# Performance work log

Measured on AMD Instinct MI355X. Metric: run time of the kernel, lower is better.

## Reference

```python
import jax, jax.numpy as jnp
import numpy as np

B, N, C, L, E = 8, 8192, 256, 4, 131072  # graphs, nodes/graph, channels (in=hidden=out), layers, edges/graph


def setup_inputs() -> dict:
    key = jax.random.key(0)
    ks = jax.random.split(key, 9)
    batch_node_tsr = jax.random.normal(ks[0], (B, N, C), jnp.float32)
    edge_index = jax.random.randint(ks[1], (B, 2, E), 0, N, jnp.int32)
    batch_last_node_idx_list = jnp.arange(1, B + 1, dtype=jnp.int32) * N - 1
    s1 = 1.0 / np.sqrt(C)
    s2 = 1.0 / np.sqrt(2 * C)
    # Base GraphConv layers: out = x @ Wr.T + sum_nbr(x) @ Wn.T + b  (all CxC since in=hidden=out)
    base_Wr = jax.random.uniform(ks[2], (L, C, C), jnp.float32, -s1, s1)
    base_Wn = jax.random.uniform(ks[3], (L, C, C), jnp.float32, -s1, s1)
    base_b = jax.random.uniform(ks[4], (L, C), jnp.float32, -s1, s1)
    # Adapter GraphConv layers take concatenated (2C) input
    adapt_Wr = jax.random.uniform(ks[5], (L, C, 2 * C), jnp.float32, -s2, s2)
    adapt_Wn = jax.random.uniform(ks[6], (L, C, 2 * C), jnp.float32, -s2, s2)
    adapt_b = jax.random.uniform(ks[7], (L, C), jnp.float32, -s2, s2)
    return dict(batch_node_tsr=batch_node_tsr, base_Wr=base_Wr, base_Wn=base_Wn,
                base_b=base_b, adapt_Wr=adapt_Wr, adapt_Wn=adapt_Wn, adapt_b=adapt_b,
                edge_index=edge_index, batch_last_node_idx_list=batch_last_node_idx_list)


def reference(batch_node_tsr, base_Wr, base_Wn, base_b, adapt_Wr, adapt_Wn, adapt_b,
              edge_index, batch_last_node_idx_list):
    # Batch graphs PyG-style: offset per-graph node indices into one big graph
    offsets = (jnp.arange(B, dtype=edge_index.dtype) * N)[:, None]  # [B,1]
    src = (edge_index[:, 0, :] + offsets).reshape(-1)  # [B*E]
    dst = (edge_index[:, 1, :] + offsets).reshape(-1)  # [B*E]
    x = batch_node_tsr.reshape(B * N, C)

    def gconv(h, Wr, Wn, b):
        # GraphConv: root transform + sum-aggregated neighbor transform
        agg = jax.ops.segment_sum(h[src], dst, num_segments=B * N)
        return h @ Wr.T + agg @ Wn.T + b

    # Base encoder pass, keeping all latent embeds
    lat = [x]
    for i in range(L):
        lat.append(jax.nn.relu(gconv(lat[-1], base_Wr[i], base_Wn[i], base_b[i])))
    base_batch_embed = lat[-1].reshape(B, N, C)

    # Adapter pass: concat(base_latent[i+1], curr) -> adapter GraphConv -> relu
    curr = x
    for i in range(L):
        curr = jax.nn.relu(gconv(jnp.concatenate([lat[i + 1], curr], axis=-1),
                                 adapt_Wr[i], adapt_Wn[i], adapt_b[i]))
    adapter_batch_embed = curr.reshape(B, N, C)
    return base_batch_embed, adapter_batch_embed
```

## Files before the change

kernel.cpp:

```cpp
#include <hip/hip_runtime.h>

#define B_ 8
#define N_ 8192
#define C_ 256
#define L_ 4
#define E_ 131072
#define BN_ 65536
#define EDGES_ 1048576
#define NKEY_ (BN_ * 4)

typedef __attribute__((ext_vector_type(8))) short short8;
typedef __attribute__((ext_vector_type(4))) float f32x4;

__device__ __forceinline__ unsigned short f2bf(float f){
  unsigned int u = __builtin_bit_cast(unsigned int, f);
  u += 0x7fffu + ((u >> 16) & 1u);
  return (unsigned short)(u >> 16);
}
__device__ __forceinline__ float bf2f(unsigned short h){
  unsigned int u = ((unsigned int)h) << 16;
  return __builtin_bit_cast(float, u);
}

__launch_bounds__(256)
__global__ void cvt_bf16_k(const float* __restrict__ in, unsigned short* __restrict__ out, int n4){
  int t = blockIdx.x * 256 + threadIdx.x;
  if (t >= n4) return;
  float4 v = ((const float4*)in)[t];
  ushort4 o;
  o.x = f2bf(v.x); o.y = f2bf(v.y); o.z = f2bf(v.z); o.w = f2bf(v.w);
  ((ushort4*)out)[t] = o;
}

__launch_bounds__(256)
__global__ void hist_k(const int* __restrict__ ei, int* __restrict__ cnt){
  int t = blockIdx.x * 256 + threadIdx.x;
  int b = t >> 17, e = t & (E_ - 1);
  int src = ei[b * (2 * E_) + e];
  int dst = ei[b * (2 * E_) + E_ + e];
  int key = (((b << 13) + dst) << 2) | (src >> 11);
  atomicAdd(&cnt[key], 1);
}

__launch_bounds__(256)
__global__ void scanA_k(const int* __restrict__ cnt, int* __restrict__ bsum){
  __shared__ int ls[256];
  int b = blockIdx.x, t = threadIdx.x;
  int4 v = *(const int4*)(cnt + b * 1024 + t * 4);
  int s = v.x + v.y + v.z + v.w;
  ls[t] = s;
  __syncthreads();
  for (int d = 128; d > 0; d >>= 1){
    if (t < d) ls[t] += ls[t + d];
    __syncthreads();
  }
  if (t == 0) bsum[b] = ls[0];
}
__launch_bounds__(256)
__global__ void scanB_k(const int* __restrict__ bsum, int* __restrict__ boff){
  __shared__ int ls[256];
  int t = threadIdx.x;
  int v = bsum[t];
  ls[t] = v;
  __syncthreads();
  for (int d = 1; d < 256; d <<= 1){
    int x = (t >= d) ? ls[t - d] : 0;
    __syncthreads();
    ls[t] += x;
    __syncthreads();
  }
  boff[t] = ls[t] - v;
}
__launch_bounds__(256)
__global__ void scanC_k(const int* __restrict__ cnt, const int* __restrict__ boff,
                        int* __restrict__ row_ptr, int* __restrict__ cursor){
  __shared__ int ls[256];
  int b = blockIdx.x, t = threadIdx.x;
  int base = b * 1024 + t * 4;
  int4 v = *(const int4*)(cnt + base);
  int s = v.x + v.y + v.z + v.w;
  ls[t] = s;
  __syncthreads();
  for (int d = 1; d < 256; d <<= 1){
    int x = (t >= d) ? ls[t - d] : 0;
    __syncthreads();
    ls[t] += x;
    __syncthreads();
  }
  int off = boff[b] + ls[t] - s;
  int4 rp;
  rp.x = off;
  rp.y = off + v.x;
  rp.z = rp.y + v.y;
  rp.w = rp.z + v.z;
  *(int4*)(row_ptr + base) = rp;
  *(int4*)(cursor + base) = rp;
  if (b == 255 && t == 255) row_ptr[NKEY_] = EDGES_;
}

__launch_bounds__(256)
__global__ void scat_k(const int* __restrict__ ei, int* __restrict__ cursor, int* __restrict__ col){
  int t = blockIdx.x * 256 + threadIdx.x;
  int b = t >> 17, e = t & (E_ - 1);
  int src = ei[b * (2 * E_) + e];
  int dst = ei[b * (2 * E_) + E_ + e];
  int key = (((b << 13) + dst) << 2) | (src >> 11);
  int pos = atomicAdd(&cursor[key], 1);
  col[pos] = (b << 13) + src;
}

__launch_bounds__(256)
__global__ void agg_k(const unsigned short* __restrict__ feat, const int* __restrict__ row_ptr,
                      const int* __restrict__ col, unsigned short* __restrict__ out){
  int w = threadIdx.x >> 6, lane = threadIdx.x & 63;
  int g = blockIdx.x & 7, sblk = blockIdx.x >> 3;
  int node = (g << 13) + (sblk << 2) + w;
  int beg = row_ptr[node << 2], end = row_ptr[(node << 2) + 4];
  int ch = lane << 2;
  float a0=0,a1=0,a2=0,a3=0;
  int e = beg;
  for (; e + 4 <= end; e += 4){
    int s0 = col[e], s1 = col[e+1], s2 = col[e+2], s3 = col[e+3];
    ushort4 v0 = *(const ushort4*)(feat + ((size_t)s0 << 8) + ch);
    ushort4 v1 = *(const ushort4*)(feat + ((size_t)s1 << 8) + ch);
    ushort4 v2 = *(const ushort4*)(feat + ((size_t)s2 << 8) + ch);
    ushort4 v3 = *(const ushort4*)(feat + ((size_t)s3 << 8) + ch);
    a0 += (bf2f(v0.x) + bf2f(v1.x)) + (bf2f(v2.x) + bf2f(v3.x));
    a1 += (bf2f(v0.y) + bf2f(v1.y)) + (bf2f(v2.y) + bf2f(v3.y));
    a2 += (bf2f(v0.z) + bf2f(v1.z)) + (bf2f(v2.z) + bf2f(v3.z));
    a3 += (bf2f(v0.w) + bf2f(v1.w)) + (bf2f(v2.w) + bf2f(v3.w));
  }
  for (; e < end; ++e){
    int s0 = col[e];
    ushort4 v0 = *(const ushort4*)(feat + ((size_t)s0 << 8) + ch);
    a0 += bf2f(v0.x); a1 += bf2f(v0.y); a2 += bf2f(v0.z); a3 += bf2f(v0.w);
  }
  ushort4 o;
  o.x = f2bf(a0); o.y = f2bf(a1); o.z = f2bf(a2); o.w = f2bf(a3);
  *(ushort4*)(out + ((size_t)node << 8) + ch) = o;
}

__launch_bounds__(256)
__global__ void agg2_k(const unsigned short* __restrict__ fA, const unsigned short* __restrict__ fB,
                       const int* __restrict__ row_ptr, const int* __restrict__ col,
                       unsigned short* __restrict__ oA, unsigned short* __restrict__ oB){
  int w = threadIdx.x >> 6, lane = threadIdx.x & 63;
  int g = blockIdx.x & 7, sblk = blockIdx.x >> 3;
  int node = (g << 13) + (sblk << 2) + w;
  int beg = row_ptr[node << 2], end = row_ptr[(node << 2) + 4];
  int ch = lane << 2;
  float a0=0,a1=0,a2=0,a3=0, c0=0,c1=0,c2=0,c3=0;
  int e = beg;
  for (; e + 4 <= end; e += 4){
    int s0 = col[e], s1 = col[e+1], s2 = col[e+2], s3 = col[e+3];
    ushort4 va0 = *(const ushort4*)(fA + ((size_t)s0 << 8) + ch);
    ushort4 va1 = *(const ushort4*)(fA + ((size_t)s1 << 8) + ch);
    ushort4 va2 = *(const ushort4*)(fA + ((size_t)s2 << 8) + ch);
    ushort4 va3 = *(const ushort4*)(fA + ((size_t)s3 << 8) + ch);
    ushort4 vb0 = *(const ushort4*)(fB + ((size_t)s0 << 8) + ch);
    ushort4 vb1 = *(const ushort4*)(fB + ((size_t)s1 << 8) + ch);
    ushort4 vb2 = *(const ushort4*)(fB + ((size_t)s2 << 8) + ch);
    ushort4 vb3 = *(const ushort4*)(fB + ((size_t)s3 << 8) + ch);
    a0 += (bf2f(va0.x) + bf2f(va1.x)) + (bf2f(va2.x) + bf2f(va3.x));
    a1 += (bf2f(va0.y) + bf2f(va1.y)) + (bf2f(va2.y) + bf2f(va3.y));
    a2 += (bf2f(va0.z) + bf2f(va1.z)) + (bf2f(va2.z) + bf2f(va3.z));
    a3 += (bf2f(va0.w) + bf2f(va1.w)) + (bf2f(va2.w) + bf2f(va3.w));
    c0 += (bf2f(vb0.x) + bf2f(vb1.x)) + (bf2f(vb2.x) + bf2f(vb3.x));
    c1 += (bf2f(vb0.y) + bf2f(vb1.y)) + (bf2f(vb2.y) + bf2f(vb3.y));
    c2 += (bf2f(vb0.z) + bf2f(vb1.z)) + (bf2f(vb2.z) + bf2f(vb3.z));
    c3 += (bf2f(vb0.w) + bf2f(vb1.w)) + (bf2f(vb2.w) + bf2f(vb3.w));
  }
  for (; e < end; ++e){
    int s0 = col[e];
    ushort4 va0 = *(const ushort4*)(fA + ((size_t)s0 << 8) + ch);
    ushort4 vb0 = *(const ushort4*)(fB + ((size_t)s0 << 8) + ch);
    a0 += bf2f(va0.x); a1 += bf2f(va0.y); a2 += bf2f(va0.z); a3 += bf2f(va0.w);
    c0 += bf2f(vb0.x); c1 += bf2f(vb0.y); c2 += bf2f(vb0.z); c3 += bf2f(vb0.w);
  }
  ushort4 oa, ob;
  oa.x = f2bf(a0); oa.y = f2bf(a1); oa.z = f2bf(a2); oa.w = f2bf(a3);
  ob.x = f2bf(c0); ob.y = f2bf(c1); ob.z = f2bf(c2); ob.w = f2bf(c3);
  *(ushort4*)(oA + ((size_t)node << 8) + ch) = oa;
  *(ushort4*)(oB + ((size_t)node << 8) + ch) = ob;
}

#define GLDS16(gp, lp) __builtin_amdgcn_global_load_lds( \
    (const __attribute__((address_space(1))) void*)(gp), \
    (__attribute__((address_space(3))) void*)(lp), 16, 0, 0)

template<int P>
__launch_bounds__(256)
__global__ void gemm_k(const unsigned short* __restrict__ A0, const unsigned short* __restrict__ A1,
                       const unsigned short* __restrict__ A2, const unsigned short* __restrict__ A3,
                       const unsigned short* __restrict__ W0, const unsigned short* __restrict__ W1,
                       const unsigned short* __restrict__ W2, const unsigned short* __restrict__ W3,
                       int ldw, const float* __restrict__ bias,
                       unsigned short* __restrict__ outb, float* __restrict__ outf){
  __shared__ unsigned short lds_u[24576];
  const unsigned short* As[4] = {A0, A1, A2, A3};
  const unsigned short* Ws[4] = {W0, W1, W2, W3};
  const int m0 = blockIdx.x << 7;
  const int t = threadIdx.x, lane = t & 63;
  const int w = t >> 6;
  const int lrow = lane & 15, kg = lane >> 4;
  f32x4 acc[2][16] = {};
  int cur = 0;

#pragma unroll
  for (int p = 0; p < P; ++p){
    const unsigned short* A = As[p] + (size_t)m0 * C_;
    const unsigned short* W = Ws[p];
    {
      unsigned short* a_t = lds_u + cur * 12288;
      unsigned short* b_t = a_t + 4096;
#pragma unroll
      for (int c = t; c < 512; c += 256){
        int row = c >> 2, seg = c & 3;
        GLDS16(A + row * C_  + seg * 8, &a_t[c * 8]);
      }
#pragma unroll
      for (int c = t; c < 1024; c += 256){
        int row = c >> 2, seg = c & 3;
        GLDS16(W + row * ldw + seg * 8, &b_t[c * 8]);
      }
      asm volatile("s_waitcnt vmcnt(0)" ::: "memory");
      __builtin_amdgcn_s_barrier();
    }
    for (int ks = 0; ks < 8; ++ks){
      if (ks < 7){
        int k0 = (ks + 1) << 5;
        unsigned short* a_t = lds_u + (cur ^ 1) * 12288;
        unsigned short* b_t = a_t + 4096;
#pragma unroll
        for (int c = t; c < 512; c += 256){
          int row = c >> 2, seg = c & 3;
          GLDS16(A + row * C_  + k0 + seg * 8, &a_t[c * 8]);
        }
#pragma unroll
        for (int c = t; c < 1024; c += 256){
          int row = c >> 2, seg = c & 3;
          GLDS16(W + row * ldw + k0 + seg * 8, &b_t[c * 8]);
        }
      }
      {
        const unsigned short* a_t = lds_u + cur * 12288;
        const unsigned short* b_t = a_t + 4096;
        short8 af[2];
#pragma unroll
        for (int m = 0; m < 2; ++m)
          af[m] = *(const short8*)&a_t[((w << 5) + (m << 4) + lrow) * 32 + (kg << 3)];
#pragma unroll
        for (int h = 0; h < 2; ++h){
          short8 bfr[8];
#pragma unroll
          for (int n2 = 0; n2 < 8; ++n2)
            bfr[n2] = *(const short8*)&b_t[((h << 7) + (n2 << 4) + lrow) * 32 + (kg << 3)];
#pragma unroll
          for (int m = 0; m < 2; ++m)
#pragma unroll
            for (int n2 = 0; n2 < 8; ++n2)
              acc[m][(h << 3) + n2] =
                  __builtin_amdgcn_mfma_f32_16x16x32_bf16(af[m], bfr[n2], acc[m][(h << 3) + n2], 0, 0, 0);
        }
      }
      asm volatile("s_waitcnt vmcnt(0)" ::: "memory");
      __builtin_amdgcn_s_barrier();
      cur ^= 1;
    }
  }
  float bv[16];
#pragma unroll
  for (int n = 0; n < 16; ++n) bv[n] = bias[(n << 4) + lrow];
  unsigned short* ep  = lds_u + (w << 11);
  float*          epf = (float*)(&lds_u[8192]) + (w << 11);
#pragma unroll
  for (int m = 0; m < 2; ++m){
    const int gr = m0 + (w << 5) + (m << 4);
    if (outf){
#pragma unroll
      for (int h = 0; h < 2; ++h){
#pragma unroll
        for (int n2 = 0; n2 < 8; ++n2){
          int n = (h << 3) + n2;
#pragma unroll
          for (int j = 0; j < 4; ++j){
            float v = acc[m][n][j] + bv[n];
            v = v > 0.f ? v : 0.f;
            epf[((kg << 2) + j) * 128 + (n2 << 4) + lrow] = v;
          }
        }
#pragma unroll
        for (int k = 0; k < 8; ++k){
          int r = (lane >> 5) + (k << 1);
          float4 v = *(const float4*)&epf[r * 128 + (lane & 31) * 4];
          *(float4*)&outf[(size_t)(gr + r) * C_ + (h << 7) + (lane & 31) * 4] = v;
        }
      }
    }
    if (outb){
#pragma unroll
      for (int h = 0; h < 2; ++h){
#pragma unroll
        for (int n2 = 0; n2 < 8; ++n2){
          int n = (h << 3) + n2;
#pragma unroll
          for (int j = 0; j < 4; ++j){
            float v = acc[m][n][j] + bv[n];
            v = v > 0.f ? v : 0.f;
            ep[((kg << 2) + j) * 128 + (n2 << 4) + lrow] = f2bf(v);
          }
        }
#pragma unroll
        for (int k = 0; k < 4; ++k){
          int r = (lane >> 4) + (k << 2);
          short8 v = *(const short8*)&ep[r * 128 + (lane & 15) * 8];
          *(short8*)&outb[(size_t)(gr + r) * C_ + (h << 7) + (lane & 15) * 8] = v;
        }
      }
    }
  }
}

extern "C" void kernel_launch(void* const* d_in, const int* in_sizes, int n_in,
                              void* d_out, int out_size, void* d_ws, size_t ws_size,
                              hipStream_t stream){
  const float* x_f   = (const float*)d_in[0];
  const float* bWr_f = (const float*)d_in[1];
  const float* bWn_f = (const float*)d_in[2];
  const float* bB    = (const float*)d_in[3];
  const float* aWr_f = (const float*)d_in[4];
  const float* aWn_f = (const float*)d_in[5];
  const float* aB    = (const float*)d_in[6];
  const int*   ei    = (const int*)d_in[7];
  float* out = (float*)d_out;
  (void)in_sizes; (void)n_in; (void)out_size; (void)ws_size;

  char* p = (char*)d_ws;
  const size_t BUF = (size_t)BN_ * C_ * sizeof(unsigned short);
  auto alloc = [&](size_t bytes){ void* r = (void*)p; p += (bytes + 255) & ~(size_t)255; return r; };
  unsigned short* xb   = (unsigned short*)alloc(BUF);
  unsigned short* latA = (unsigned short*)alloc(BUF);
  unsigned short* latB = (unsigned short*)alloc(BUF);
  unsigned short* curA = (unsigned short*)alloc(BUF);
  unsigned short* curB = (unsigned short*)alloc(BUF);
  unsigned short* agg0 = (unsigned short*)alloc(BUF);
  unsigned short* agg1 = (unsigned short*)alloc(BUF);
  unsigned short* wbR  = (unsigned short*)alloc((size_t)L_ * C_ * C_ * 2);
  unsigned short* wbN  = (unsigned short*)alloc((size_t)L_ * C_ * C_ * 2);
  unsigned short* waR  = (unsigned short*)alloc((size_t)L_ * C_ * 2 * C_ * 2);
  unsigned short* waN  = (unsigned short*)alloc((size_t)L_ * C_ * 2 * C_ * 2);
  int* cnt     = (int*)alloc((size_t)NKEY_ * 4);
  int* row_ptr = (int*)alloc((size_t)(NKEY_ + 1) * 4);
  int* cursor  = (int*)alloc((size_t)NKEY_ * 4);
  int* colx    = (int*)alloc((size_t)EDGES_ * 4);
  int* bsum    = (int*)alloc(256 * 4);
  int* boff    = (int*)alloc(256 * 4);

  cvt_bf16_k<<<BN_ * C_ / 4 / 256, 256, 0, stream>>>(x_f, xb, BN_ * C_ / 4);
  cvt_bf16_k<<<L_ * C_ * C_ / 4 / 256, 256, 0, stream>>>(bWr_f, wbR, L_ * C_ * C_ / 4);
  cvt_bf16_k<<<L_ * C_ * C_ / 4 / 256, 256, 0, stream>>>(bWn_f, wbN, L_ * C_ * C_ / 4);
  cvt_bf16_k<<<L_ * C_ * 2 * C_ / 4 / 256, 256, 0, stream>>>(aWr_f, waR, L_ * C_ * 2 * C_ / 4);
  cvt_bf16_k<<<L_ * C_ * 2 * C_ / 4 / 256, 256, 0, stream>>>(aWn_f, waN, L_ * C_ * 2 * C_ / 4);

  hipMemsetAsync(cnt, 0, (size_t)NKEY_ * 4, stream);
  hist_k<<<EDGES_ / 256, 256, 0, stream>>>(ei, cnt);
  scanA_k<<<256, 256, 0, stream>>>(cnt, bsum);
  scanB_k<<<1, 256, 0, stream>>>(bsum, boff);
  scanC_k<<<256, 256, 0, stream>>>(cnt, boff, row_ptr, cursor);
  scat_k<<<EDGES_ / 256, 256, 0, stream>>>(ei, cursor, colx);

  const int AGG_GRID  = BN_ / 4;
  const int GEMM_GRID = BN_ / 128;

  const size_t WB = (size_t)C_ * C_;
  const size_t WA = (size_t)C_ * 2 * C_;

  agg_k<<<AGG_GRID, 256, 0, stream>>>(xb, row_ptr, colx, agg0);
  gemm_k<2><<<GEMM_GRID, 256, 0, stream>>>(xb, agg0, nullptr, nullptr,
      wbR, wbN, nullptr, nullptr, C_, bB, latA, nullptr);
  agg_k<<<AGG_GRID, 256, 0, stream>>>(latA, row_ptr, colx, agg1);
  gemm_k<2><<<GEMM_GRID, 256, 0, stream>>>(latA, agg1, nullptr, nullptr,
      wbR + WB, wbN + WB, nullptr, nullptr, C_, bB + 256, latB, nullptr);
  gemm_k<4><<<GEMM_GRID, 256, 0, stream>>>(latA, xb, agg1, agg0,
      waR, waR + 256, waN, waN + 256, 2 * C_, aB, curA, nullptr);
  agg2_k<<<AGG_GRID, 256, 0, stream>>>(latB, curA, row_ptr, colx, agg1, agg0);
  gemm_k<2><<<GEMM_GRID, 256, 0, stream>>>(latB, agg1, nullptr, nullptr,
      wbR + 2 * WB, wbN + 2 * WB, nullptr, nullptr, C_, bB + 512, latA, nullptr);
  gemm_k<4><<<GEMM_GRID, 256, 0, stream>>>(latB, curA, agg1, agg0,
      waR + WA, waR + WA + 256, waN + WA, waN + WA + 256, 2 * C_, aB + 256, curB, nullptr);
  agg2_k<<<AGG_GRID, 256, 0, stream>>>(latA, curB, row_ptr, colx, agg1, agg0);
  gemm_k<2><<<GEMM_GRID, 256, 0, stream>>>(latA, agg1, nullptr, nullptr,
      wbR + 3 * WB, wbN + 3 * WB, nullptr, nullptr, C_, bB + 768, latB, out);
  gemm_k<4><<<GEMM_GRID, 256, 0, stream>>>(latA, curB, agg1, agg0,
      waR + 2 * WA, waR + 2 * WA + 256, waN + 2 * WA, waN + 2 * WA + 256, 2 * C_, aB + 512, curA, nullptr);
  agg2_k<<<AGG_GRID, 256, 0, stream>>>(latB, curA, row_ptr, colx, agg1, agg0);
  gemm_k<4><<<GEMM_GRID, 256, 0, stream>>>(latB, curA, agg1, agg0,
      waR + 3 * WA, waR + 3 * WA + 256, waN + 3 * WA, waN + 3 * WA + 256, 2 * C_, aB + 768,
      nullptr, out + (size_t)BN_ * C_);
}
```

Measured before the change: 1.103 ms.

## Pipeline GEMM K-loop across passes, swizzle LDS tiles, nontemporal agg loads/stores

Result: slower. 1.152 ms (+4.5%).

```diff
diff --git a/kernel.cpp b/kernel.cpp
--- a/kernel.cpp
+++ b/kernel.cpp
@@ -120,7 +120,10 @@
   float a0=0,a1=0,a2=0,a3=0;
   int e = beg;
   for (; e + 4 <= end; e += 4){
-    int s0 = col[e], s1 = col[e+1], s2 = col[e+2], s3 = col[e+3];
+    int s0 = __builtin_nontemporal_load(col + e);
+    int s1 = __builtin_nontemporal_load(col + e + 1);
+    int s2 = __builtin_nontemporal_load(col + e + 2);
+    int s3 = __builtin_nontemporal_load(col + e + 3);
     ushort4 v0 = *(const ushort4*)(feat + ((size_t)s0 << 8) + ch);
     ushort4 v1 = *(const ushort4*)(feat + ((size_t)s1 << 8) + ch);
     ushort4 v2 = *(const ushort4*)(feat + ((size_t)s2 << 8) + ch);
@@ -131,13 +134,14 @@
     a3 += (bf2f(v0.w) + bf2f(v1.w)) + (bf2f(v2.w) + bf2f(v3.w));
   }
   for (; e < end; ++e){
-    int s0 = col[e];
+    int s0 = __builtin_nontemporal_load(col + e);
     ushort4 v0 = *(const ushort4*)(feat + ((size_t)s0 << 8) + ch);
     a0 += bf2f(v0.x); a1 += bf2f(v0.y); a2 += bf2f(v0.z); a3 += bf2f(v0.w);
   }
   ushort4 o;
   o.x = f2bf(a0); o.y = f2bf(a1); o.z = f2bf(a2); o.w = f2bf(a3);
-  *(ushort4*)(out + ((size_t)node << 8) + ch) = o;
+  unsigned long long ov = __builtin_bit_cast(unsigned long long, o);
+  __builtin_nontemporal_store(ov, (unsigned long long*)(out + ((size_t)node << 8) + ch));
 }
 
 __launch_bounds__(256)
@@ -151,27 +155,20 @@
   int ch = lane << 2;
   float a0=0,a1=0,a2=0,a3=0, c0=0,c1=0,c2=0,c3=0;
   int e = beg;
-  for (; e + 4 <= end; e += 4){
-    int s0 = col[e], s1 = col[e+1], s2 = col[e+2], s3 = col[e+3];
+  for (; e + 2 <= end; e += 2){
+    int s0 = __builtin_nontemporal_load(col + e);
+    int s1 = __builtin_nontemporal_load(col + e + 1);
     ushort4 va0 = *(const ushort4*)(fA + ((size_t)s0 << 8) + ch);
+    ushort4 vb0 = *(const ushort4*)(fB + ((size_t)s0 << 8) + ch);
     ushort4 va1 = *(const ushort4*)(fA + ((size_t)s1 << 8) + ch);
-    ushort4 va2 = *(const ushort4*)(fA + ((size_t)s2 << 8) + ch);
-    ushort4 va3 = *(const ushort4*)(fA + ((size_t)s3 << 8) + ch);
-    ushort4 vb0 = *(const ushort4*)(fB + ((size_t)s0 << 8) + ch);
     ushort4 vb1 = *(const ushort4*)(fB + ((size_t)s1 << 8) + ch);
-    ushort4 vb2 = *(const ushort4*)(fB + ((size_t)s2 << 8) + ch);
-    ushort4 vb3 = *(const ushort4*)(fB + ((size_t)s3 << 8) + ch);
-    a0 += (bf2f(va0.x) + bf2f(va1.x)) + (bf2f(va2.x) + bf2f(va3.x));
-    a1 += (bf2f(va0.y) + bf2f(va1.y)) + (bf2f(va2.y) + bf2f(va3.y));
-    a2 += (bf2f(va0.z) + bf2f(va1.z)) + (bf2f(va2.z) + bf2f(va3.z));
-    a3 += (bf2f(va0.w) + bf2f(va1.w)) + (bf2f(va2.w) + bf2f(va3.w));
-    c0 += (bf2f(vb0.x) + bf2f(vb1.x)) + (bf2f(vb2.x) + bf2f(vb3.x));
-    c1 += (bf2f(vb0.y) + bf2f(vb1.y)) + (bf2f(vb2.y) + bf2f(vb3.y));
-    c2 += (bf2f(vb0.z) + bf2f(vb1.z)) + (bf2f(vb2.z) + bf2f(vb3.z));
-    c3 += (bf2f(vb0.w) + bf2f(vb1.w)) + (bf2f(vb2.w) + bf2f(vb3.w));
-  }
-  for (; e < end; ++e){
-    int s0 = col[e];
+    a0 += bf2f(va0.x) + bf2f(va1.x); a1 += bf2f(va0.y) + bf2f(va1.y);
+    a2 += bf2f(va0.z) + bf2f(va1.z); a3 += bf2f(va0.w) + bf2f(va1.w);
+    c0 += bf2f(vb0.x) + bf2f(vb1.x); c1 += bf2f(vb0.y) + bf2f(vb1.y);
+    c2 += bf2f(vb0.z) + bf2f(vb1.z); c3 += bf2f(vb0.w) + bf2f(vb1.w);
+  }
+  if (e < end){
+    int s0 = __builtin_nontemporal_load(col + e);
     ushort4 va0 = *(const ushort4*)(fA + ((size_t)s0 << 8) + ch);
     ushort4 vb0 = *(const ushort4*)(fB + ((size_t)s0 << 8) + ch);
     a0 += bf2f(va0.x); a1 += bf2f(va0.y); a2 += bf2f(va0.z); a3 += bf2f(va0.w);
@@ -180,13 +177,33 @@
   ushort4 oa, ob;
   oa.x = f2bf(a0); oa.y = f2bf(a1); oa.z = f2bf(a2); oa.w = f2bf(a3);
   ob.x = f2bf(c0); ob.y = f2bf(c1); ob.z = f2bf(c2); ob.w = f2bf(c3);
-  *(ushort4*)(oA + ((size_t)node << 8) + ch) = oa;
-  *(ushort4*)(oB + ((size_t)node << 8) + ch) = ob;
+  unsigned long long va = __builtin_bit_cast(unsigned long long, oa);
+  unsigned long long vb = __builtin_bit_cast(unsigned long long, ob);
+  __builtin_nontemporal_store(va, (unsigned long long*)(oA + ((size_t)node << 8) + ch));
+  __builtin_nontemporal_store(vb, (unsigned long long*)(oB + ((size_t)node << 8) + ch));
 }
 
 #define GLDS16(gp, lp) __builtin_amdgcn_global_load_lds( \
     (const __attribute__((address_space(1))) void*)(gp), \
     (__attribute__((address_space(3))) void*)(lp), 16, 0, 0)
+
+__device__ __forceinline__ void stage_tiles(const unsigned short* __restrict__ A,
+                                            const unsigned short* __restrict__ W,
+                                            int ldw, int k0, unsigned short* a_t, int t){
+  unsigned short* b_t = a_t + 4096;
+#pragma unroll
+  for (int c = t; c < 512; c += 256){
+    int row = c >> 2, seg = c & 3;
+    int sg = seg ^ ((row >> 1) & 3);
+    GLDS16(A + row * C_  + k0 + sg * 8, &a_t[c * 8]);
+  }
+#pragma unroll
+  for (int c = t; c < 1024; c += 256){
+    int row = c >> 2, seg = c & 3;
+    int sg = seg ^ ((row >> 1) & 3);
+    GLDS16(W + row * ldw + k0 + sg * 8, &b_t[c * 8]);
+  }
+}
 
 template<int P>
 __launch_bounds__(256)
@@ -204,68 +221,47 @@
   const int w = t >> 6;
   const int lrow = lane & 15, kg = lane >> 4;
   f32x4 acc[2][16] = {};
-  int cur = 0;
-
+
+  stage_tiles(As[0] + (size_t)m0 * C_, Ws[0], ldw, 0, lds_u, t);
 #pragma unroll
   for (int p = 0; p < P; ++p){
     const unsigned short* A = As[p] + (size_t)m0 * C_;
     const unsigned short* W = Ws[p];
-    {
-      unsigned short* a_t = lds_u + cur * 12288;
-      unsigned short* b_t = a_t + 4096;
-#pragma unroll
-      for (int c = t; c < 512; c += 256){
-        int row = c >> 2, seg = c & 3;
-        GLDS16(A + row * C_  + seg * 8, &a_t[c * 8]);
+#pragma unroll
+    for (int ks = 0; ks < 8; ++ks){
+      const int par = ks & 1;
+      const bool more = (ks < 7) || (p + 1 < P);
+      if (ks < 7)
+        stage_tiles(A, W, ldw, (ks + 1) << 5, lds_u + (par ^ 1) * 12288, t);
+      else if (p + 1 < P)
+        stage_tiles(As[p + 1] + (size_t)m0 * C_, Ws[p + 1], ldw, 0, lds_u + (par ^ 1) * 12288, t);
+      if (more) asm volatile("s_waitcnt vmcnt(6)" ::: "memory");
+      else      asm volatile("s_waitcnt vmcnt(0)" ::: "memory");
+      __builtin_amdgcn_s_barrier();
+      const unsigned short* a_t = lds_u + par * 12288;
+      const unsigned short* b_t = a_t + 4096;
+      short8 af[2];
+#pragma unroll
+      for (int m = 0; m < 2; ++m){
+        int ra = (w << 5) + (m << 4) + lrow;
+        af[m] = *(const short8*)&a_t[ra * 32 + ((kg ^ ((ra >> 1) & 3)) << 3)];
       }
 #pragma unroll
-      for (int c = t; c < 1024; c += 256){
-        int row = c >> 2, seg = c & 3;
-        GLDS16(W + row * ldw + seg * 8, &b_t[c * 8]);
+      for (int h = 0; h < 2; ++h){
+        short8 bfr[8];
+#pragma unroll
+        for (int n2 = 0; n2 < 8; ++n2){
+          int rb = (h << 7) + (n2 << 4) + lrow;
+          bfr[n2] = *(const short8*)&b_t[rb * 32 + ((kg ^ ((rb >> 1) & 3)) << 3)];
+        }
+#pragma unroll
+        for (int m = 0; m < 2; ++m)
+#pragma unroll
+          for (int n2 = 0; n2 < 8; ++n2)
+            acc[m][(h << 3) + n2] =
+                __builtin_amdgcn_mfma_f32_16x16x32_bf16(af[m], bfr[n2], acc[m][(h << 3) + n2], 0, 0, 0);
       }
-      asm volatile("s_waitcnt vmcnt(0)" ::: "memory");
       __builtin_amdgcn_s_barrier();
-    }
-    for (int ks = 0; ks < 8; ++ks){
-      if (ks < 7){
-        int k0 = (ks + 1) << 5;
-        unsigned short* a_t = lds_u + (cur ^ 1) * 12288;
-        unsigned short* b_t = a_t + 4096;
-#pragma unroll
-        for (int c = t; c < 512; c += 256){
-          int row = c >> 2, seg = c & 3;
-          GLDS16(A + row * C_  + k0 + seg * 8, &a_t[c * 8]);
-        }
-#pragma unroll
-        for (int c = t; c < 1024; c += 256){
-          int row = c >> 2, seg = c & 3;
-          GLDS16(W + row * ldw + k0 + seg * 8, &b_t[c * 8]);
-        }
-      }
-      {
-        const unsigned short* a_t = lds_u + cur * 12288;
-        const unsigned short* b_t = a_t + 4096;
-        short8 af[2];
-#pragma unroll
-        for (int m = 0; m < 2; ++m)
-          af[m] = *(const short8*)&a_t[((w << 5) + (m << 4) + lrow) * 32 + (kg << 3)];
-#pragma unroll
-        for (int h = 0; h < 2; ++h){
-          short8 bfr[8];
-#pragma unroll
-          for (int n2 = 0; n2 < 8; ++n2)
-            bfr[n2] = *(const short8*)&b_t[((h << 7) + (n2 << 4) + lrow) * 32 + (kg << 3)];
-#pragma unroll
-          for (int m = 0; m < 2; ++m)
-#pragma unroll
-            for (int n2 = 0; n2 < 8; ++n2)
-              acc[m][(h << 3) + n2] =
-                  __builtin_amdgcn_mfma_f32_16x16x32_bf16(af[m], bfr[n2], acc[m][(h << 3) + n2], 0, 0, 0);
-        }
-      }
-      asm volatile("s_waitcnt vmcnt(0)" ::: "memory");
-      __builtin_amdgcn_s_barrier();
-      cur ^= 1;
     }
   }
   float bv[16];
```
